# Performance work log

Measured on AMD Instinct MI355X. Metric: run time of the kernel, lower is better.

## Reference

```python
import jax, jax.numpy as jnp
import numpy as np

N = 100000
E = 1600000
C_IN = 32
C_OUT = 64
B = 4
VOXEL_SIZE = 0.0625
GRID_LO, GRID_HI = 0.0, 1.0
VOX = int((GRID_HI - GRID_LO) / VOXEL_SIZE)  # 16
R_CORR = GRID_HI - GRID_LO  # r_correction = max(grid_scale) - min(grid_scale) = 1


def setup_inputs() -> dict:
    key = jax.random.key(0)
    k1, k2, k3, k4, k5, k6 = jax.random.split(key, 6)
    x = jax.random.normal(k1, (N, C_IN), dtype=jnp.float32)
    edge_index = jax.random.randint(k2, (2, E), 0, N, dtype=jnp.int32)
    pos = jax.random.uniform(k3, (N, 2), dtype=jnp.float32)
    batch = jnp.sort(jax.random.randint(k4, (N,), 0, B, dtype=jnp.int32))
    W = jax.random.normal(k5, (C_OUT, 4 * C_IN), dtype=jnp.float32) / np.sqrt(4 * C_IN)
    b = jax.random.normal(k6, (C_OUT,), dtype=jnp.float32) * 0.01
    return {"x": x, "edge_index": edge_index, "pos": pos, "batch": batch, "W": W, "b": b}


def dpo_conv(x, edge_index, pos, W, b):
    row, col = edge_index[0], edge_index[1]  # j = source, i = target (PyG default flow)
    pos_i, pos_j = pos[col], pos[row]        # [E, 2]
    v_i, v_j = x[col], x[row]                # [E, C_IN]
    diff = pos_i - pos_j                     # [E, 2]
    r2 = jnp.sum(diff * diff, axis=1, keepdims=True)  # [E, 1]
    w = diff * R_CORR / (r2 + 0.01)          # [E, 2] -> columns are diff_x, diff_y
    v_diff = v_i - v_j                       # [E, C_IN]
    # message f: [E, 3*C_IN]
    f = jnp.concatenate([v_diff * w[:, 0:1], v_diff * w[:, 1:2], v_j], axis=1)
    # scatter-mean into target nodes i = col
    summed = jax.ops.segment_sum(f, col, num_segments=N)            # [N, 3*C_IN]
    cnt = jax.ops.segment_sum(jnp.ones((E, 1), f.dtype), col, num_segments=N)
    prop = summed / jnp.maximum(cnt, 1.0)
    prop = jnp.concatenate([prop, x], axis=1)  # [N, 4*C_IN]
    return prop @ W.T + b


def reference(x, edge_index, pos, batch, W, b):
    h = jax.nn.relu(dpo_conv(x, edge_index, pos, W, b))  # [N, C_OUT]
    # voxel_grid: per-graph voxel cluster ids, then max_pool per cluster (dense grid)
    vox = jnp.clip(jnp.floor((pos - GRID_LO) / VOXEL_SIZE).astype(jnp.int32), 0, VOX - 1)
    cluster = batch * (VOX * VOX) + vox[:, 1] * VOX + vox[:, 0]     # [N]
    n_clusters = B * VOX * VOX
    pooled_x = jax.ops.segment_max(h, cluster, num_segments=n_clusters)  # [B*V^2, C_OUT]
    pooled_x = jnp.where(jnp.isfinite(pooled_x), pooled_x, 0.0)          # empty voxels -> 0
    pos_sum = jax.ops.segment_sum(pos, cluster, num_segments=n_clusters)
    node_cnt = jax.ops.segment_sum(jnp.ones((N, 1), pos.dtype), cluster, num_segments=n_clusters)
    pooled_pos = pos_sum / jnp.maximum(node_cnt, 1.0)                    # mean pos per voxel
    return pooled_x, pooled_pos, pos, batch
```

## Files before the change

### kernel.cpp

```cpp
#include <hip/hip_runtime.h>
#include <hip/hip_fp16.h>

#define NN 100000
#define NE 1600000
#define NCLUST 1024
#define OUT_POOLED_POS 65536
#define OUT_POS        67584
#define OUT_BATCH      267584
#define ZROW ((unsigned)NN)

static __device__ __forceinline__ float2 h2f(unsigned int u)
{
    __half2 h = *reinterpret_cast<__half2*>(&u);
    return __half22float2(h);
}

__global__ __launch_bounds__(256) void cvt_kernel(const float4* __restrict__ x4,
                                                  uint2* __restrict__ xh2)
{
    int t = blockIdx.x * 256 + threadIdx.x;
    if (t >= NN * 8) return;
    float4 v = x4[t];
    __half2 lo = __floats2half2_rn(v.x, v.y);
    __half2 hi = __floats2half2_rn(v.z, v.w);
    uint2 o;
    o.x = *reinterpret_cast<unsigned int*>(&lo);
    o.y = *reinterpret_cast<unsigned int*>(&hi);
    xh2[t] = o;
}

__global__ __launch_bounds__(256) void fill_kernel(const int* __restrict__ ei,
                                                   const float2* __restrict__ pos2,
                                                   int* __restrict__ wp,
                                                   uint2* __restrict__ csr64,
                                                   int cap)
{
    int t = blockIdx.x * 256 + threadIdx.x;
    int e0 = t * 4;
    if (e0 + 3 < NE) {
        int4 r = *(const int4*)(ei + e0);
        int4 c = *(const int4*)(ei + NE + e0);
        int rr[4] = {r.x, r.y, r.z, r.w};
        int cc[4] = {c.x, c.y, c.z, c.w};
        #pragma unroll
        for (int u = 0; u < 4; ++u) {
            int row = rr[u], col = cc[u];
            float2 pi = pos2[col], pj = pos2[row];
            float dx = pi.x - pj.x, dy = pi.y - pj.y;
            float inv = __builtin_amdgcn_rcpf(dx * dx + dy * dy + 0.01f);
            __half2 h2 = __floats2half2_rn(dx * inv, dy * inv);
            unsigned int wbits = *reinterpret_cast<unsigned int*>(&h2);
            int s = atomicAdd(&wp[col], 1);
            if (s < cap) csr64[(size_t)s * NN + col] = make_uint2((unsigned)row, wbits);
        }
    } else {
        for (int e = e0; e < NE; ++e) {
            int row = ei[e], col = ei[NE + e];
            float2 pi = pos2[col], pj = pos2[row];
            float dx = pi.x - pj.x, dy = pi.y - pj.y;
            float inv = __builtin_amdgcn_rcpf(dx * dx + dy * dy + 0.01f);
            __half2 h2 = __floats2half2_rn(dx * inv, dy * inv);
            unsigned int wbits = *reinterpret_cast<unsigned int*>(&h2);
            int s = atomicAdd(&wp[col], 1);
            if (s < cap) csr64[(size_t)s * NN + col] = make_uint2((unsigned)row, wbits);
        }
    }
}

__global__ __launch_bounds__(1024, 8) void fused_kernel(
    const float2* __restrict__ xf2,
    const unsigned int* __restrict__ xh32,
    const float2* __restrict__ pos2,
    const int* __restrict__ batch,
    const float4* __restrict__ W4,
    const float* __restrict__ bv,
    const int* __restrict__ wp,
    const uint2* __restrict__ csr64,
    int cap,
    float* __restrict__ out,
    float* __restrict__ pos_sum,
    float* __restrict__ node_cnt)
{
    __shared__ float4 Wt4[32 * 64];
    __shared__ float  bs[64];
    __shared__ float4 prop4[16][4][32];

    {
        int oc0 = threadIdx.x & 63;
        int k0  = threadIdx.x >> 6;
        Wt4[k0 * 64 + oc0]        = W4[oc0 * 32 + k0];
        Wt4[(k0 + 16) * 64 + oc0] = W4[oc0 * 32 + k0 + 16];
        if (threadIdx.x < 64) bs[threadIdx.x] = bv[threadIdx.x];
    }
    __syncthreads();

    const int wid  = threadIdx.x >> 6;
    const int lane = threadIdx.x & 63;
    const int q  = lane >> 4;
    const int s  = lane & 15;
    const int oc = lane;
    const int nwaves = gridDim.x * 16;
    const uint2 ZE = make_uint2(ZROW, 0u);

    for (int wg = blockIdx.x * 16 + wid; wg * 4 < NN; wg += nwaves) {
        int n = wg * 4 + q;
        bool act = (n < NN);
        int nn = act ? n : 0;

        int cnt = wp[nn];
        int deg = act ? min(cnt, cap) : 0;
        float2 vi = xf2[(size_t)nn * 16 + s];
        const uint2* bkp = csr64 + nn;

        int md = deg;
        md = max(md, __shfl_xor(md, 16));
        md = max(md, __shfl_xor(md, 32));

        float a0x = 0.f, a0y = 0.f;
        float a1x = 0.f, a1y = 0.f;
        float a2x = 0.f, a2y = 0.f;

        uint2 E0 = (0 < deg) ? bkp[(size_t)0 * NN] : ZE;
        uint2 E1 = (1 < deg) ? bkp[(size_t)1 * NN] : ZE;
        uint2 E2 = (2 < deg) ? bkp[(size_t)2 * NN] : ZE;
        uint2 E3 = (3 < deg) ? bkp[(size_t)3 * NN] : ZE;
        uint2 E4 = (4 < deg) ? bkp[(size_t)4 * NN] : ZE;
        uint2 E5 = (5 < deg) ? bkp[(size_t)5 * NN] : ZE;
        uint2 E6 = (6 < deg) ? bkp[(size_t)6 * NN] : ZE;
        uint2 E7 = (7 < deg) ? bkp[(size_t)7 * NN] : ZE;
        unsigned X0 = xh32[(size_t)E0.x * 16 + s];
        unsigned X1 = xh32[(size_t)E1.x * 16 + s];
        unsigned X2 = xh32[(size_t)E2.x * 16 + s];
        unsigned X3 = xh32[(size_t)E3.x * 16 + s];
        unsigned X4 = xh32[(size_t)E4.x * 16 + s];
        unsigned X5 = xh32[(size_t)E5.x * 16 + s];
        unsigned X6 = xh32[(size_t)E6.x * 16 + s];
        unsigned X7 = xh32[(size_t)E7.x * 16 + s];
        unsigned B0 = E0.y, B1 = E1.y, B2 = E2.y, B3 = E3.y;
        unsigned B4 = E4.y, B5 = E5.y, B6 = E6.y, B7 = E7.y;

        int kb = 0;
        int iters = (md + 7) >> 3;
        for (int it = 0; it < iters; ++it) {
            int nb = kb + 8;
            uint2 F0 = (nb     < deg) ? bkp[(size_t)(nb    ) * NN] : ZE;
            uint2 F1 = (nb + 1 < deg) ? bkp[(size_t)(nb + 1) * NN] : ZE;
            uint2 F2 = (nb + 2 < deg) ? bkp[(size_t)(nb + 2) * NN] : ZE;
            uint2 F3 = (nb + 3 < deg) ? bkp[(size_t)(nb + 3) * NN] : ZE;
            uint2 F4 = (nb + 4 < deg) ? bkp[(size_t)(nb + 4) * NN] : ZE;
            uint2 F5 = (nb + 5 < deg) ? bkp[(size_t)(nb + 5) * NN] : ZE;
            uint2 F6 = (nb + 6 < deg) ? bkp[(size_t)(nb + 6) * NN] : ZE;
            uint2 F7 = (nb + 7 < deg) ? bkp[(size_t)(nb + 7) * NN] : ZE;

            #define EDGE(Bi, Xi)                                              \
            {                                                                 \
                float2 w = h2f(Bi), v = h2f(Xi);                              \
                float vdx = vi.x - v.x, vdy = vi.y - v.y;                     \
                a0x += vdx * w.x; a0y += vdy * w.x;                           \
                a1x += vdx * w.y; a1y += vdy * w.y;                           \
                a2x += v.x;       a2y += v.y;                                 \
            }
            EDGE(B0, X0) EDGE(B1, X1) EDGE(B2, X2) EDGE(B3, X3)
            EDGE(B4, X4) EDGE(B5, X5) EDGE(B6, X6) EDGE(B7, X7)
            #undef EDGE

            if (it + 1 < iters) {
                X0 = xh32[(size_t)F0.x * 16 + s]; B0 = F0.y;
                X1 = xh32[(size_t)F1.x * 16 + s]; B1 = F1.y;
                X2 = xh32[(size_t)F2.x * 16 + s]; B2 = F2.y;
                X3 = xh32[(size_t)F3.x * 16 + s]; B3 = F3.y;
                X4 = xh32[(size_t)F4.x * 16 + s]; B4 = F4.y;
                X5 = xh32[(size_t)F5.x * 16 + s]; B5 = F5.y;
                X6 = xh32[(size_t)F6.x * 16 + s]; B6 = F6.y;
                X7 = xh32[(size_t)F7.x * 16 + s]; B7 = F7.y;
            }
            kb = nb;
        }

        float invd = 1.0f / fmaxf((float)cnt, 1.0f);
        if (act) {
            float2* pw = (float2*)&prop4[wid][q][0];
            pw[s]      = make_float2(a0x * invd, a0y * invd);
            pw[16 + s] = make_float2(a1x * invd, a1y * invd);
            pw[32 + s] = make_float2(a2x * invd, a2y * invd);
            pw[48 + s] = vi;
        }
        asm volatile("s_waitcnt lgkmcnt(0)" ::: "memory");

        float bb = bs[oc];
        float acc0 = bb, acc1 = bb, acc2 = bb, acc3 = bb;
        #pragma unroll 8
        for (int k4 = 0; k4 < 32; ++k4) {
            float4 w   = Wt4[k4 * 64 + oc];
            float4 pp0 = prop4[wid][0][k4];
            float4 pp1 = prop4[wid][1][k4];
            float4 pp2 = prop4[wid][2][k4];
            float4 pp3 = prop4[wid][3][k4];
            acc0 += w.x*pp0.x + w.y*pp0.y + w.z*pp0.z + w.w*pp0.w;
            acc1 += w.x*pp1.x + w.y*pp1.y + w.z*pp1.z + w.w*pp1.w;
            acc2 += w.x*pp2.x + w.y*pp2.y + w.z*pp2.z + w.w*pp2.w;
            acc3 += w.x*pp3.x + w.y*pp3.y + w.z*pp3.z + w.w*pp3.w;
        }

        float accq[4] = {acc0, acc1, acc2, acc3};
        #pragma unroll
        for (int qq = 0; qq < 4; ++qq) {
            int n2 = wg * 4 + qq;
            if (n2 < NN) {
                float h = fmaxf(accq[qq], 0.0f);
                float2 pp = pos2[n2];
                int b = batch[n2];
                int vx = min(max((int)floorf(pp.x * 16.0f), 0), 15);
                int vy = min(max((int)floorf(pp.y * 16.0f), 0), 15);
                int cl = b * 256 + vy * 16 + vx;
                unsigned int* tgt = (unsigned int*)(out + (size_t)cl * 64 + oc);
                unsigned int prev = *tgt;
                unsigned int cur  = __float_as_uint(h);
                if (cur > prev) atomicMax(tgt, cur);
                if (oc == qq) {
                    *(float2*)(out + OUT_POS + 2 * (size_t)n2) = pp;
                    out[OUT_BATCH + n2] = (float)b;
                    atomicAdd(pos_sum + 2 * cl,     pp.x);
                    atomicAdd(pos_sum + 2 * cl + 1, pp.y);
                    atomicAdd(node_cnt + cl, 1.0f);
                }
            }
        }
        asm volatile("s_waitcnt lgkmcnt(0)" ::: "memory");
    }
}

__global__ void finalize_kernel(const float* __restrict__ pos_sum,
                                const float* __restrict__ node_cnt,
                                float* __restrict__ out_pooled_pos)
{
    int c = blockIdx.x * blockDim.x + threadIdx.x;
    if (c >= NCLUST) return;
    float inv = 1.0f / fmaxf(node_cnt[c], 1.0f);
    out_pooled_pos[2 * c]     = pos_sum[2 * c] * inv;
    out_pooled_pos[2 * c + 1] = pos_sum[2 * c + 1] * inv;
}

extern "C" void kernel_launch(void* const* d_in, const int* in_sizes, int n_in,
                              void* d_out, int out_size, void* d_ws, size_t ws_size,
                              hipStream_t stream)
{
    const float* x     = (const float*)d_in[0];
    const int*   ei    = (const int*)d_in[1];
    const float* pos   = (const float*)d_in[2];
    const int*   batch = (const int*)d_in[3];
    const float* W     = (const float*)d_in[4];
    const float* bvec  = (const float*)d_in[5];
    float* out = (float*)d_out;

    size_t fixed = (size_t)NN * 4 + (size_t)(NN + 1) * 8 * 8 + 3 * NCLUST * 4;
    int cap = 40;
    if (ws_size < fixed + (size_t)NN * cap * 8) {
        cap = (int)((ws_size - fixed) / ((size_t)NN * 8));
        if (cap > 40) cap = 40;
    }

    int* wp = (int*)d_ws;
    uint2* csr64 = (uint2*)(wp + NN);
    uint2* xh2 = csr64 + (size_t)NN * cap;
    float* pos_sum  = (float*)(xh2 + (size_t)(NN + 1) * 8);
    float* node_cnt = pos_sum + 2 * NCLUST;

    hipMemsetAsync(wp, 0, NN * sizeof(int), stream);
    hipMemsetAsync(xh2 + (size_t)NN * 8, 0, 64, stream);
    hipMemsetAsync(pos_sum, 0, 3 * NCLUST * sizeof(float), stream);
    hipMemsetAsync(d_out, 0, (size_t)NCLUST * 64 * sizeof(float), stream);

    cvt_kernel<<<(NN * 8 + 255) / 256, 256, 0, stream>>>((const float4*)x, xh2);

    fill_kernel<<<(NE / 4 + 255) / 256, 256, 0, stream>>>(
        ei, (const float2*)pos, wp, csr64, cap);

    fused_kernel<<<512, 1024, 0, stream>>>(
        (const float2*)x, (const unsigned int*)xh2, (const float2*)pos, batch,
        (const float4*)W, bvec, wp, csr64, cap, out, pos_sum, node_cnt);

    finalize_kernel<<<(NCLUST + 255) / 256, 256, 0, stream>>>(
        pos_sum, node_cnt, out + NCLUST * 64);
}
```

Baseline: 300.1 us.

## Switch CSR buffer to node-major layout and stage neighbor lists in LDS

```diff
diff --git a/kernel.cpp b/kernel.cpp
--- a/kernel.cpp
+++ b/kernel.cpp
@@ -51,7 +51,7 @@
             __half2 h2 = __floats2half2_rn(dx * inv, dy * inv);
             unsigned int wbits = *reinterpret_cast<unsigned int*>(&h2);
             int s = atomicAdd(&wp[col], 1);
-            if (s < cap) csr64[(size_t)s * NN + col] = make_uint2((unsigned)row, wbits);
+            if (s < cap) csr64[(size_t)col * cap + s] = make_uint2((unsigned)row, wbits);
         }
     } else {
         for (int e = e0; e < NE; ++e) {
@@ -62,7 +62,7 @@
             __half2 h2 = __floats2half2_rn(dx * inv, dy * inv);
             unsigned int wbits = *reinterpret_cast<unsigned int*>(&h2);
             int s = atomicAdd(&wp[col], 1);
-            if (s < cap) csr64[(size_t)s * NN + col] = make_uint2((unsigned)row, wbits);
+            if (s < cap) csr64[(size_t)col * cap + s] = make_uint2((unsigned)row, wbits);
         }
     }
 }
@@ -110,7 +110,19 @@
         int cnt = wp[nn];
         int deg = act ? min(cnt, cap) : 0;
         float2 vi = xf2[(size_t)nn * 16 + s];
-        const uint2* bkp = csr64 + nn;
+
+        uint2* bq = (uint2*)&prop4[wid][q][0];
+        {
+            const uint2* src = csr64 + (size_t)nn * cap;
+            #pragma unroll
+            for (int r = 0; r < 3; ++r) {
+                int k = r * 16 + s;
+                uint2 e = (k < deg) ? src[k] : ZE;
+                bq[k] = e;
+            }
+        }
+        asm volatile("s_waitcnt lgkmcnt(0)" ::: "memory");
+        const uint4* bq4 = (const uint4*)bq;
 
         int md = deg;
         md = max(md, __shfl_xor(md, 16));
@@ -120,62 +132,60 @@
         float a1x = 0.f, a1y = 0.f;
         float a2x = 0.f, a2y = 0.f;
 
-        uint2 E0 = (0 < deg) ? bkp[(size_t)0 * NN] : ZE;
-        uint2 E1 = (1 < deg) ? bkp[(size_t)1 * NN] : ZE;
-        uint2 E2 = (2 < deg) ? bkp[(size_t)2 * NN] : ZE;
-        uint2 E3 = (3 < deg) ? bkp[(size_t)3 * NN] : ZE;
-        uint2 E4 = (4 < deg) ? bkp[(size_t)4 * NN] : ZE;
-        uint2 E5 = (5 < deg) ? bkp[(size_t)5 * NN] : ZE;
-        uint2 E6 = (6 < deg) ? bkp[(size_t)6 * NN] : ZE;
-        uint2 E7 = (7 < deg) ? bkp[(size_t)7 * NN] : ZE;
-        unsigned X0 = xh32[(size_t)E0.x * 16 + s];
-        unsigned X1 = xh32[(size_t)E1.x * 16 + s];
-        unsigned X2 = xh32[(size_t)E2.x * 16 + s];
-        unsigned X3 = xh32[(size_t)E3.x * 16 + s];
-        unsigned X4 = xh32[(size_t)E4.x * 16 + s];
-        unsigned X5 = xh32[(size_t)E5.x * 16 + s];
-        unsigned X6 = xh32[(size_t)E6.x * 16 + s];
-        unsigned X7 = xh32[(size_t)E7.x * 16 + s];
-        unsigned B0 = E0.y, B1 = E1.y, B2 = E2.y, B3 = E3.y;
-        unsigned B4 = E4.y, B5 = E5.y, B6 = E6.y, B7 = E7.y;
-
-        int kb = 0;
+        unsigned Xa0,Xa1,Xa2,Xa3,Xa4,Xa5,Xa6,Xa7;
+        unsigned Ba0,Ba1,Ba2,Ba3,Ba4,Ba5,Ba6,Ba7;
+        unsigned Xb0,Xb1,Xb2,Xb3,Xb4,Xb5,Xb6,Xb7;
+        unsigned Bb0,Bb1,Bb2,Bb3,Bb4,Bb5,Bb6,Bb7;
+
+        #define ISSUE(base, X0_,B0_,X1_,B1_,X2_,B2_,X3_,B3_,X4_,B4_,X5_,B5_,X6_,B6_,X7_,B7_) { \
+            uint4 e0 = bq4[((base) >> 1) + 0];                                \
+            uint4 e1 = bq4[((base) >> 1) + 1];                                \
+            uint4 e2 = bq4[((base) >> 1) + 2];                                \
+            uint4 e3 = bq4[((base) >> 1) + 3];                                \
+            X0_ = xh32[(size_t)e0.x * 16 + s]; B0_ = e0.y;                    \
+            X1_ = xh32[(size_t)e0.z * 16 + s]; B1_ = e0.w;                    \
+            X2_ = xh32[(size_t)e1.x * 16 + s]; B2_ = e1.y;                    \
+            X3_ = xh32[(size_t)e1.z * 16 + s]; B3_ = e1.w;                    \
+            X4_ = xh32[(size_t)e2.x * 16 + s]; B4_ = e2.y;                    \
+            X5_ = xh32[(size_t)e2.z * 16 + s]; B5_ = e2.w;                    \
+            X6_ = xh32[(size_t)e3.x * 16 + s]; B6_ = e3.y;                    \
+            X7_ = xh32[(size_t)e3.z * 16 + s]; B7_ = e3.w;                    \
+        }
+
+        #define EDGE(Bi, Xi) {                                                \
+            float2 w = h2f(Bi), v = h2f(Xi);                                  \
+            float vdx = vi.x - v.x, vdy = vi.y - v.y;                         \
+            a0x += vdx * w.x; a0y += vdy * w.x;                               \
+            a1x += vdx * w.y; a1y += vdy * w.y;                               \
+            a2x += v.x;       a2y += v.y;                                     \
+        }
+        #define COMPUTE8(P) EDGE(B##P##0, X##P##0) EDGE(B##P##1, X##P##1)     \
+                            EDGE(B##P##2, X##P##2) EDGE(B##P##3, X##P##3)     \
+                            EDGE(B##P##4, X##P##4) EDGE(B##P##5, X##P##5)     \
+                            EDGE(B##P##6, X##P##6) EDGE(B##P##7, X##P##7)
+
         int iters = (md + 7) >> 3;
-        for (int it = 0; it < iters; ++it) {
-            int nb = kb + 8;
-            uint2 F0 = (nb     < deg) ? bkp[(size_t)(nb    ) * NN] : ZE;
-            uint2 F1 = (nb + 1 < deg) ? bkp[(size_t)(nb + 1) * NN] : ZE;
-            uint2 F2 = (nb + 2 < deg) ? bkp[(size_t)(nb + 2) * NN] : ZE;
-            uint2 F3 = (nb + 3 < deg) ? bkp[(size_t)(nb + 3) * NN] : ZE;
-            uint2 F4 = (nb + 4 < deg) ? bkp[(size_t)(nb + 4) * NN] : ZE;
-            uint2 F5 = (nb + 5 < deg) ? bkp[(size_t)(nb + 5) * NN] : ZE;
-            uint2 F6 = (nb + 6 < deg) ? bkp[(size_t)(nb + 6) * NN] : ZE;
-            uint2 F7 = (nb + 7 < deg) ? bkp[(size_t)(nb + 7) * NN] : ZE;
-
-            #define EDGE(Bi, Xi)                                              \
-            {                                                                 \
-                float2 w = h2f(Bi), v = h2f(Xi);                              \
-                float vdx = vi.x - v.x, vdy = vi.y - v.y;                     \
-                a0x += vdx * w.x; a0y += vdy * w.x;                           \
-                a1x += vdx * w.y; a1y += vdy * w.y;                           \
-                a2x += v.x;       a2y += v.y;                                 \
+        ISSUE(0, Xa0,Ba0,Xa1,Ba1,Xa2,Ba2,Xa3,Ba3,Xa4,Ba4,Xa5,Ba5,Xa6,Ba6,Xa7,Ba7)
+        int kb = 0, it = 0;
+        if (iters > 0) {
+            while (true) {
+                bool more = (it + 1 < iters);
+                if (more)
+                    ISSUE(kb + 8, Xb0,Bb0,Xb1,Bb1,Xb2,Bb2,Xb3,Bb3,Xb4,Bb4,Xb5,Bb5,Xb6,Bb6,Xb7,Bb7)
+                COMPUTE8(a)
+                ++it; kb += 8;
+                if (!more) break;
+                bool more2 = (it + 1 < iters);
+                if (more2)
+                    ISSUE(kb + 8, Xa0,Ba0,Xa1,Ba1,Xa2,Ba2,Xa3,Ba3,Xa4,Ba4,Xa5,Ba5,Xa6,Ba6,Xa7,Ba7)
+                COMPUTE8(b)
+                ++it; kb += 8;
+                if (!more2) break;
             }
-            EDGE(B0, X0) EDGE(B1, X1) EDGE(B2, X2) EDGE(B3, X3)
-            EDGE(B4, X4) EDGE(B5, X5) EDGE(B6, X6) EDGE(B7, X7)
-            #undef EDGE
-
-            if (it + 1 < iters) {
-                X0 = xh32[(size_t)F0.x * 16 + s]; B0 = F0.y;
-                X1 = xh32[(size_t)F1.x * 16 + s]; B1 = F1.y;
-                X2 = xh32[(size_t)F2.x * 16 + s]; B2 = F2.y;
-                X3 = xh32[(size_t)F3.x * 16 + s]; B3 = F3.y;
-                X4 = xh32[(size_t)F4.x * 16 + s]; B4 = F4.y;
-                X5 = xh32[(size_t)F5.x * 16 + s]; B5 = F5.y;
-                X6 = xh32[(size_t)F6.x * 16 + s]; B6 = F6.y;
-                X7 = xh32[(size_t)F7.x * 16 + s]; B7 = F7.y;
-            }
-            kb = nb;
-        }
+        }
+        #undef COMPUTE8
+        #undef EDGE
+        #undef ISSUE
 
         float invd = 1.0f / fmaxf((float)cnt, 1.0f);
         if (act) {
```

Result: faster. 293.3 us (-2.3%).

## Store CSR buckets node-major and deepen gather prefetch to two stages

Applied to the files above, without the earlier changes.

```diff
diff --git a/kernel.cpp b/kernel.cpp
--- a/kernel.cpp
+++ b/kernel.cpp
@@ -51,7 +51,7 @@
             __half2 h2 = __floats2half2_rn(dx * inv, dy * inv);
             unsigned int wbits = *reinterpret_cast<unsigned int*>(&h2);
             int s = atomicAdd(&wp[col], 1);
-            if (s < cap) csr64[(size_t)s * NN + col] = make_uint2((unsigned)row, wbits);
+            if (s < cap) csr64[(size_t)col * cap + s] = make_uint2((unsigned)row, wbits);
         }
     } else {
         for (int e = e0; e < NE; ++e) {
@@ -62,12 +62,12 @@
             __half2 h2 = __floats2half2_rn(dx * inv, dy * inv);
             unsigned int wbits = *reinterpret_cast<unsigned int*>(&h2);
             int s = atomicAdd(&wp[col], 1);
-            if (s < cap) csr64[(size_t)s * NN + col] = make_uint2((unsigned)row, wbits);
-        }
-    }
-}
-
-__global__ __launch_bounds__(1024, 8) void fused_kernel(
+            if (s < cap) csr64[(size_t)col * cap + s] = make_uint2((unsigned)row, wbits);
+        }
+    }
+}
+
+__global__ __launch_bounds__(1024, 4) void fused_kernel(
     const float2* __restrict__ xf2,
     const unsigned int* __restrict__ xh32,
     const float2* __restrict__ pos2,
@@ -110,7 +110,7 @@
         int cnt = wp[nn];
         int deg = act ? min(cnt, cap) : 0;
         float2 vi = xf2[(size_t)nn * 16 + s];
-        const uint2* bkp = csr64 + nn;
+        const uint2* bk = csr64 + (size_t)nn * cap;
 
         int md = deg;
         md = max(md, __shfl_xor(md, 16));
@@ -120,61 +120,45 @@
         float a1x = 0.f, a1y = 0.f;
         float a2x = 0.f, a2y = 0.f;
 
-        uint2 E0 = (0 < deg) ? bkp[(size_t)0 * NN] : ZE;
-        uint2 E1 = (1 < deg) ? bkp[(size_t)1 * NN] : ZE;
-        uint2 E2 = (2 < deg) ? bkp[(size_t)2 * NN] : ZE;
-        uint2 E3 = (3 < deg) ? bkp[(size_t)3 * NN] : ZE;
-        uint2 E4 = (4 < deg) ? bkp[(size_t)4 * NN] : ZE;
-        uint2 E5 = (5 < deg) ? bkp[(size_t)5 * NN] : ZE;
-        uint2 E6 = (6 < deg) ? bkp[(size_t)6 * NN] : ZE;
-        uint2 E7 = (7 < deg) ? bkp[(size_t)7 * NN] : ZE;
-        unsigned X0 = xh32[(size_t)E0.x * 16 + s];
-        unsigned X1 = xh32[(size_t)E1.x * 16 + s];
-        unsigned X2 = xh32[(size_t)E2.x * 16 + s];
-        unsigned X3 = xh32[(size_t)E3.x * 16 + s];
-        unsigned X4 = xh32[(size_t)E4.x * 16 + s];
-        unsigned X5 = xh32[(size_t)E5.x * 16 + s];
-        unsigned X6 = xh32[(size_t)E6.x * 16 + s];
-        unsigned X7 = xh32[(size_t)E7.x * 16 + s];
-        unsigned B0 = E0.y, B1 = E1.y, B2 = E2.y, B3 = E3.y;
-        unsigned B4 = E4.y, B5 = E5.y, B6 = E6.y, B7 = E7.y;
-
-        int kb = 0;
+        uint2    En[8];
+        unsigned Xc[8], Wc[8];
+        unsigned Xn[8], Wn[8];
+
+        #pragma unroll
+        for (int u = 0; u < 8; ++u) En[u] = (u < deg) ? bk[u] : ZE;
+        #pragma unroll
+        for (int u = 0; u < 8; ++u) {
+            Xc[u] = xh32[(size_t)En[u].x * 16 + s];
+            Wc[u] = En[u].y;
+        }
+        #pragma unroll
+        for (int u = 0; u < 8; ++u) En[u] = (8 + u < deg) ? bk[8 + u] : ZE;
+
         int iters = (md + 7) >> 3;
         for (int it = 0; it < iters; ++it) {
-            int nb = kb + 8;
-            uint2 F0 = (nb     < deg) ? bkp[(size_t)(nb    ) * NN] : ZE;
-            uint2 F1 = (nb + 1 < deg) ? bkp[(size_t)(nb + 1) * NN] : ZE;
-            uint2 F2 = (nb + 2 < deg) ? bkp[(size_t)(nb + 2) * NN] : ZE;
-            uint2 F3 = (nb + 3 < deg) ? bkp[(size_t)(nb + 3) * NN] : ZE;
-            uint2 F4 = (nb + 4 < deg) ? bkp[(size_t)(nb + 4) * NN] : ZE;
-            uint2 F5 = (nb + 5 < deg) ? bkp[(size_t)(nb + 5) * NN] : ZE;
-            uint2 F6 = (nb + 6 < deg) ? bkp[(size_t)(nb + 6) * NN] : ZE;
-            uint2 F7 = (nb + 7 < deg) ? bkp[(size_t)(nb + 7) * NN] : ZE;
-
-            #define EDGE(Bi, Xi)                                              \
-            {                                                                 \
-                float2 w = h2f(Bi), v = h2f(Xi);                              \
-                float vdx = vi.x - v.x, vdy = vi.y - v.y;                     \
-                a0x += vdx * w.x; a0y += vdy * w.x;                           \
-                a1x += vdx * w.y; a1y += vdy * w.y;                           \
-                a2x += v.x;       a2y += v.y;                                 \
-            }
-            EDGE(B0, X0) EDGE(B1, X1) EDGE(B2, X2) EDGE(B3, X3)
-            EDGE(B4, X4) EDGE(B5, X5) EDGE(B6, X6) EDGE(B7, X7)
-            #undef EDGE
-
             if (it + 1 < iters) {
-                X0 = xh32[(size_t)F0.x * 16 + s]; B0 = F0.y;
-                X1 = xh32[(size_t)F1.x * 16 + s]; B1 = F1.y;
-                X2 = xh32[(size_t)F2.x * 16 + s]; B2 = F2.y;
-                X3 = xh32[(size_t)F3.x * 16 + s]; B3 = F3.y;
-                X4 = xh32[(size_t)F4.x * 16 + s]; B4 = F4.y;
-                X5 = xh32[(size_t)F5.x * 16 + s]; B5 = F5.y;
-                X6 = xh32[(size_t)F6.x * 16 + s]; B6 = F6.y;
-                X7 = xh32[(size_t)F7.x * 16 + s]; B7 = F7.y;
-            }
-            kb = nb;
+                #pragma unroll
+                for (int u = 0; u < 8; ++u) {
+                    Xn[u] = xh32[(size_t)En[u].x * 16 + s];
+                    Wn[u] = En[u].y;
+                }
+            }
+            if (it + 2 < iters) {
+                int b2 = (it + 2) * 8;
+                #pragma unroll
+                for (int u = 0; u < 8; ++u)
+                    En[u] = (b2 + u < deg) ? bk[b2 + u] : ZE;
+            }
+            #pragma unroll
+            for (int u = 0; u < 8; ++u) {
+                float2 w = h2f(Wc[u]), v = h2f(Xc[u]);
+                float vdx = vi.x - v.x, vdy = vi.y - v.y;
+                a0x += vdx * w.x; a0y += vdy * w.x;
+                a1x += vdx * w.y; a1y += vdy * w.y;
+                a2x += v.x;       a2y += v.y;
+            }
+            #pragma unroll
+            for (int u = 0; u < 8; ++u) { Xc[u] = Xn[u]; Wc[u] = Wn[u]; }
         }
 
         float invd = 1.0f / fmaxf((float)cnt, 1.0f);
```

Result: faster. 282.9 us (-5.7%).
